# Kernel tuning notes

Measured on AMD Instinct MI355X. Metric: run time of the kernel, lower is better.

## Reference

```python
import jax, jax.numpy as jnp
import numpy as np

N = 50000
IN_CH = 64
HID_CH = 32
NEG_SLOPE = 0.2  # PyG GATConv default for attention LeakyReLU


def _glorot(key, shape):
    fan = shape[0] + shape[-1] if len(shape) > 1 else shape[0]
    s = jnp.sqrt(6.0 / fan)
    return jax.random.uniform(key, shape, jnp.float32, -s, s)


def setup_inputs() -> dict:
    key = jax.random.key(0)
    ks = jax.random.split(key, 20)
    x = jax.random.normal(ks[0], (N, IN_CH), jnp.float32)
    edge_index = jax.random.randint(ks[1], (2, 800000), 0, N, jnp.int64)
    dims = [(IN_CH, IN_CH), (IN_CH, HID_CH), (HID_CH, IN_CH), (IN_CH, IN_CH)]
    inp = {"x": x, "edge_index": edge_index}
    for i, (di, do) in enumerate(dims, 1):
        inp[f"w{i}"] = _glorot(ks[4 * i - 2], (di, do))
        inp[f"as{i}"] = _glorot(ks[4 * i - 1], (do,))
        inp[f"ad{i}"] = _glorot(ks[4 * i], (do,))
        inp[f"b{i}"] = jnp.zeros((do,), jnp.float32)
    return inp


def _gat_layer(x, src, dst, W, a_src, a_dst, b):
    # x: [N, di] -> h: [N, do]
    h = x @ W
    # per-edge attention logits (source + destination contributions)
    e = jax.nn.leaky_relu(h[src] @ a_src + h[dst] @ a_dst, NEG_SLOPE)  # [E]
    # numerically stable segment softmax over incoming edges per dst node
    m = jax.ops.segment_max(e, dst, num_segments=N)
    ex = jnp.exp(e - m[dst])
    denom = jax.ops.segment_sum(ex, dst, num_segments=N)
    alpha = ex / (denom[dst] + 1e-16)  # [E]
    out = jax.ops.segment_sum(alpha[:, None] * h[src], dst, num_segments=N)
    return out + b


def reference(x, edge_index, w1, as1, ad1, b1, w2, as2, ad2, b2,
              w3, as3, ad3, b3, w4, as4, ad4, b4):
    # PyG GATConv adds self-loops by default
    ar = jnp.arange(N, dtype=edge_index.dtype)
    src = jnp.concatenate([edge_index[0], ar])
    dst = jnp.concatenate([edge_index[1], ar])

    h1 = jax.nn.relu(_gat_layer(x, src, dst, w1, as1, ad1, b1))
    h = _gat_layer(h1, src, dst, w2, as2, ad2, b2)
    h3 = jax.nn.relu(h)
    h4 = jax.nn.relu(_gat_layer(h3, src, dst, w3, as3, ad3, b3))
    out = _gat_layer(h4, src, dst, w4, as4, ad4, b4)
    return (out, h)
```

## Files before the change

kernel.cpp:

```cpp
#include <hip/hip_runtime.h>
#include <hip/hip_fp16.h>
#include <math.h>

#define N_NODES 50000
#define N_EDGES 800000
#define E_TOT   850000
#define NEG_SLOPE 0.2f
#define NB_SCAN 49

__global__ void csr_init(int* deg) {
    int i = blockIdx.x * blockDim.x + threadIdx.x;
    if (i < N_NODES) deg[i] = 0;
}

__global__ void csr_degree(const int* __restrict__ dst, int* __restrict__ deg,
                           int* __restrict__ rank) {
    int e = blockIdx.x * blockDim.x + threadIdx.x;
    if (e >= E_TOT) return;
    int d = (e < N_EDGES) ? dst[e] : (e - N_EDGES);
    rank[e] = atomicAdd(&deg[d], 1);
}

__global__ void scan_p1(const int* __restrict__ deg, int* __restrict__ bsum) {
    __shared__ int red[1024];
    int i = blockIdx.x * 1024 + threadIdx.x;
    red[threadIdx.x] = (i < N_NODES) ? deg[i] : 0;
    __syncthreads();
    for (int off = 512; off >= 1; off >>= 1) {
        if (threadIdx.x < off) red[threadIdx.x] += red[threadIdx.x + off];
        __syncthreads();
    }
    if (threadIdx.x == 0) bsum[blockIdx.x] = red[0];
}

__global__ void scan_p3(const int* __restrict__ deg, const int* __restrict__ bsum,
                        int* __restrict__ offs) {
    __shared__ int s[1024];
    __shared__ int bofs;
    int i = blockIdx.x * 1024 + threadIdx.x;
    int v = (i < N_NODES) ? deg[i] : 0;
    s[threadIdx.x] = v;
    if (threadIdx.x < 64) {
        int d = (threadIdx.x < NB_SCAN) ? bsum[threadIdx.x] : 0;
        int p = d;
        for (int off = 1; off < 64; off <<= 1) {
            int u = __shfl_up(p, off, 64);
            if ((int)threadIdx.x >= off) p += u;
        }
        if ((int)threadIdx.x == (int)blockIdx.x) bofs = p - d;
        if (blockIdx.x == NB_SCAN - 1 && threadIdx.x == NB_SCAN - 1)
            offs[N_NODES] = p;
    }
    __syncthreads();
    for (int off = 1; off < 1024; off <<= 1) {
        int u = (threadIdx.x >= off) ? s[threadIdx.x - off] : 0;
        __syncthreads();
        s[threadIdx.x] += u;
        __syncthreads();
    }
    if (i < N_NODES) offs[i] = bofs + s[threadIdx.x] - v;
}

__global__ void csr_fill(const int* __restrict__ src, const int* __restrict__ dst,
                         const int* __restrict__ rank, const int* __restrict__ offs,
                         int* __restrict__ csr_src) {
    int e = blockIdx.x * blockDim.x + threadIdx.x;
    if (e >= E_TOT) return;
    int s, d;
    if (e < N_EDGES) { s = src[e]; d = dst[e]; } else { s = e - N_EDGES; d = s; }
    csr_src[offs[d] + rank[e]] = s;
}

template<int DI, int DO>
__global__ void gemm_proj(const float* __restrict__ X, const float* __restrict__ W,
                          const float* __restrict__ a_src, const float* __restrict__ a_dst,
                          __half* __restrict__ Hh, float* __restrict__ ssrc,
                          float* __restrict__ sdst) {
    const int TPN = DO / 4;
    const int NPB = 256 / TPN;
    __shared__ float sW[DI * DO];
    __shared__ float sX[NPB][DI + 1];
    const int tid = threadIdx.x;
    for (int i = tid; i < DI * DO / 4; i += 256)
        ((float4*)sW)[i] = ((const float4*)W)[i];
    const int base = blockIdx.x * NPB;
    for (int i = tid; i < NPB * DI; i += 256) {
        int r = i / DI, col = i % DI;
        int node = base + r;
        sX[r][col] = (node < N_NODES) ? X[(long)node * DI + col] : 0.0f;
    }
    __syncthreads();
    const int cq = tid % TPN;
    const int g  = tid / TPN;
    const int node = base + g;
    if (node >= N_NODES) return;
    float ax = 0.0f, ay = 0.0f, az = 0.0f, aw = 0.0f;
    const float4* sW4 = (const float4*)sW;
#pragma unroll
    for (int k = 0; k < DI; k++) {
        float xv = sX[g][k];
        float4 w4 = sW4[k * TPN + cq];
        ax = fmaf(xv, w4.x, ax); ay = fmaf(xv, w4.y, ay);
        az = fmaf(xv, w4.z, az); aw = fmaf(xv, w4.w, aw);
    }
    union { uint2 u; __half2 h2[2]; } pk;
    pk.h2[0] = __float22half2_rn(make_float2(ax, ay));
    pk.h2[1] = __float22half2_rn(make_float2(az, aw));
    ((uint2*)(Hh + (long)node * DO))[cq] = pk.u;

    float4 as4 = ((const float4*)a_src)[cq];
    float4 ad4 = ((const float4*)a_dst)[cq];
    float ps = ax * as4.x + ay * as4.y + az * as4.z + aw * as4.w;
    float pd = ax * ad4.x + ay * ad4.y + az * ad4.z + aw * ad4.w;
#pragma unroll
    for (int m = TPN / 2; m >= 1; m >>= 1) {
        ps += __shfl_xor(ps, m, TPN);
        pd += __shfl_xor(pd, m, TPN);
    }
    if (cq == 0) { ssrc[node] = ps; sdst[node] = pd; }
}

template<int DO>
__global__ void gather(const __half* __restrict__ Hh, const float* __restrict__ ssrc,
                       const float* __restrict__ sdst, const int* __restrict__ offs,
                       const int* __restrict__ csr_src, const float* __restrict__ bias,
                       float* __restrict__ feat_out, float* __restrict__ extra_out,
                       int do_relu) {
    const int G = DO / 4;
    const int t = threadIdx.x;
    const int node = blockIdx.x * (256 / G) + t / G;
    const int r = t % G;
    if (node >= N_NODES) return;
    const int beg = offs[node], end = offs[node + 1];
    const float sdv = sdst[node];
    const uint2* H2 = (const uint2*)Hh;

    float4 acc = make_float4(0.0f, 0.0f, 0.0f, 0.0f);
    float den = 0.0f;
    for (int cb = beg; cb < end; cb += G) {
        const int cnt = min(G, end - cb);
        int s0 = 0; float ex = 0.0f;
        if (r < cnt) {
            s0 = csr_src[cb + r];
            float v = ssrc[s0] + sdv;
            v = (v > 0.0f) ? v : NEG_SLOPE * v;
            ex = __expf(v);
        }
        den += ex;
        int j = 0;
        for (; j + 4 <= cnt; j += 4) {
            int   sa = __shfl(s0, j,     G), sb = __shfl(s0, j + 1, G);
            int   sc = __shfl(s0, j + 2, G), sd2 = __shfl(s0, j + 3, G);
            float ea = __shfl(ex, j,     G), eb = __shfl(ex, j + 1, G);
            float ec = __shfl(ex, j + 2, G), ed = __shfl(ex, j + 3, G);
            union { uint2 u; __half2 h2[2]; } ua, ub, uc, ud;
            ua.u = H2[(long)sa * G + r];
            ub.u = H2[(long)sb * G + r];
            uc.u = H2[(long)sc * G + r];
            ud.u = H2[(long)sd2 * G + r];
            float2 a0 = __half22float2(ua.h2[0]), a1 = __half22float2(ua.h2[1]);
            float2 b0 = __half22float2(ub.h2[0]), b1 = __half22float2(ub.h2[1]);
            float2 c0 = __half22float2(uc.h2[0]), c1 = __half22float2(uc.h2[1]);
            float2 d0 = __half22float2(ud.h2[0]), d1 = __half22float2(ud.h2[1]);
            acc.x = fmaf(ea, a0.x, acc.x); acc.y = fmaf(ea, a0.y, acc.y);
            acc.z = fmaf(ea, a1.x, acc.z); acc.w = fmaf(ea, a1.y, acc.w);
            acc.x = fmaf(eb, b0.x, acc.x); acc.y = fmaf(eb, b0.y, acc.y);
            acc.z = fmaf(eb, b1.x, acc.z); acc.w = fmaf(eb, b1.y, acc.w);
            acc.x = fmaf(ec, c0.x, acc.x); acc.y = fmaf(ec, c0.y, acc.y);
            acc.z = fmaf(ec, c1.x, acc.z); acc.w = fmaf(ec, c1.y, acc.w);
            acc.x = fmaf(ed, d0.x, acc.x); acc.y = fmaf(ed, d0.y, acc.y);
            acc.z = fmaf(ed, d1.x, acc.z); acc.w = fmaf(ed, d1.y, acc.w);
        }
        for (; j < cnt; j++) {
            int   sa = __shfl(s0, j, G);
            float ea = __shfl(ex, j, G);
            union { uint2 u; __half2 h2[2]; } ua;
            ua.u = H2[(long)sa * G + r];
            float2 a0 = __half22float2(ua.h2[0]), a1 = __half22float2(ua.h2[1]);
            acc.x = fmaf(ea, a0.x, acc.x); acc.y = fmaf(ea, a0.y, acc.y);
            acc.z = fmaf(ea, a1.x, acc.z); acc.w = fmaf(ea, a1.y, acc.w);
        }
    }
#pragma unroll
    for (int m = G / 2; m >= 1; m >>= 1) den += __shfl_xor(den, m, G);

    float inv = 1.0f / (den + 1e-16f);
    float4 b4 = ((const float4*)bias)[r];
    float4 o;
    o.x = acc.x * inv + b4.x; o.y = acc.y * inv + b4.y;
    o.z = acc.z * inv + b4.z; o.w = acc.w * inv + b4.w;
    long idx = (long)node * G + r;
    if (extra_out) ((float4*)extra_out)[idx] = o;
    if (feat_out) {
        if (do_relu) {
            o.x = fmaxf(o.x, 0.0f); o.y = fmaxf(o.y, 0.0f);
            o.z = fmaxf(o.z, 0.0f); o.w = fmaxf(o.w, 0.0f);
        }
        ((float4*)feat_out)[idx] = o;
    }
}

template<int DI, int DO>
static void run_layer(const float* in_feat, const float* W, const float* a_src,
                      const float* a_dst, const float* b, int do_relu,
                      __half* Hh, float* SS, float* SD,
                      const int* offs, const int* csr_src,
                      float* feat_out, float* extra_out, hipStream_t stream) {
    const int TPN = DO / 4;
    const int NPB = 256 / TPN;
    gemm_proj<DI, DO><<<(N_NODES + NPB - 1) / NPB, 256, 0, stream>>>(
        in_feat, W, a_src, a_dst, Hh, SS, SD);
    const int G = DO / 4;
    const int GNPB = 256 / G;
    gather<DO><<<(N_NODES + GNPB - 1) / GNPB, 256, 0, stream>>>(
        Hh, SS, SD, offs, csr_src, b, feat_out, extra_out, do_relu);
}

extern "C" void kernel_launch(void* const* d_in, const int* in_sizes, int n_in,
                              void* d_out, int out_size, void* d_ws, size_t ws_size,
                              hipStream_t stream) {
    const float* x  = (const float*)d_in[0];
    const int*   ei = (const int*)d_in[1];

    const float* w1  = (const float*)d_in[2];
    const float* as1 = (const float*)d_in[3];
    const float* ad1 = (const float*)d_in[4];
    const float* b1  = (const float*)d_in[5];
    const float* w2  = (const float*)d_in[6];
    const float* as2 = (const float*)d_in[7];
    const float* ad2 = (const float*)d_in[8];
    const float* b2  = (const float*)d_in[9];
    const float* w3  = (const float*)d_in[10];
    const float* as3 = (const float*)d_in[11];
    const float* ad3 = (const float*)d_in[12];
    const float* b3  = (const float*)d_in[13];
    const float* w4  = (const float*)d_in[14];
    const float* as4 = (const float*)d_in[15];
    const float* ad4 = (const float*)d_in[16];
    const float* b4  = (const float*)d_in[17];

    float* out_final = (float*)d_out;
    float* out_h     = (float*)d_out + N_NODES * 64;

    float* ws   = (float*)d_ws;
    __half* Hh  = (__half*)ws;
    float* FEAT = ws + N_NODES * 32;
    float* SS   = FEAT + N_NODES * 64;
    float* SD   = SS + N_NODES;
    int* deg     = (int*)(SD + N_NODES);
    int* rank    = deg + N_NODES;
    int* offs    = rank + E_TOT;
    int* csr_src = offs + N_NODES + 1;
    int* bsum    = csr_src + E_TOT;

    const int* src = ei;
    const int* dst = ei + N_EDGES;

    csr_init<<<(N_NODES + 255) / 256, 256, 0, stream>>>(deg);
    csr_degree<<<(E_TOT + 255) / 256, 256, 0, stream>>>(dst, deg, rank);
    scan_p1<<<NB_SCAN, 1024, 0, stream>>>(deg, bsum);
    scan_p3<<<NB_SCAN, 1024, 0, stream>>>(deg, bsum, offs);
    csr_fill<<<(E_TOT + 255) / 256, 256, 0, stream>>>(src, dst, rank, offs, csr_src);

    run_layer<64, 64>(x, w1, as1, ad1, b1, 1, Hh, SS, SD, offs, csr_src, FEAT, nullptr, stream);
    run_layer<64, 32>(FEAT, w2, as2, ad2, b2, 1, Hh, SS, SD, offs, csr_src, FEAT, out_h, stream);
    run_layer<32, 64>(FEAT, w3, as3, ad3, b3, 1, Hh, SS, SD, offs, csr_src, FEAT, nullptr, stream);
    run_layer<64, 64>(FEAT, w4, as4, ad4, b4, 0, Hh, SS, SD, offs, csr_src, nullptr, out_final, stream);
}
```

Baseline: 291.9 us.

## Fuse each layer's aggregation with the next layer's projection GEMM

Merges the gather/softmax aggregation of layer k with the dense projection and attention-score computation of layer k+1 in a single kernel. The next layer's weight matrix is staged in LDS, and the aggregated row is broadcast across the node's thread group via shuffles. This removes the fp32 intermediate feature write and re-read between layers and cuts three kernel launches. Hidden buffers are now double-buffered as fp16 plus score arrays. The cost is extra LDS use and more register pressure in the gather kernel.

```diff
diff --git a/kernel.cpp b/kernel.cpp
--- a/kernel.cpp
+++ b/kernel.cpp
@@ -120,20 +120,36 @@
     if (cq == 0) { ssrc[node] = ps; sdst[node] = pd; }
 }
 
-template<int DO>
-__global__ void gather(const __half* __restrict__ Hh, const float* __restrict__ ssrc,
-                       const float* __restrict__ sdst, const int* __restrict__ offs,
-                       const int* __restrict__ csr_src, const float* __restrict__ bias,
-                       float* __restrict__ feat_out, float* __restrict__ extra_out,
-                       int do_relu) {
-    const int G = DO / 4;
+template<int DIN, int DOUT>
+__global__ void gather_gemm(const __half* __restrict__ Hh_in,
+                            const float* __restrict__ ssrc_in,
+                            const float* __restrict__ sdst_in,
+                            const int* __restrict__ offs,
+                            const int* __restrict__ csr_src,
+                            const float* __restrict__ bias_in,
+                            int relu_o, float* __restrict__ extra_out,
+                            const float* __restrict__ W2,
+                            const float* __restrict__ a_src2,
+                            const float* __restrict__ a_dst2,
+                            __half* __restrict__ Hh_out,
+                            float* __restrict__ ssrc2, float* __restrict__ sdst2) {
+    const int G = DIN / 4;
+    const int NPB = 256 / G;
+    constexpr int LDSW = (DOUT > 0) ? DIN * DOUT : 1;
+    __shared__ float sW[LDSW];
+    if constexpr (DOUT > 0) {
+        for (int i = threadIdx.x; i < DIN * DOUT / 4; i += 256)
+            ((float4*)sW)[i] = ((const float4*)W2)[i];
+        __syncthreads();
+    }
     const int t = threadIdx.x;
-    const int node = blockIdx.x * (256 / G) + t / G;
+    const int node = blockIdx.x * NPB + t / G;
     const int r = t % G;
-    if (node >= N_NODES) return;
-    const int beg = offs[node], end = offs[node + 1];
-    const float sdv = sdst[node];
-    const uint2* H2 = (const uint2*)Hh;
+    const bool valid = (node < N_NODES);
+    const int beg = valid ? offs[node] : 0;
+    const int end = valid ? offs[node + 1] : 0;
+    const float sdv = valid ? sdst_in[node] : 0.0f;
+    const uint2* H2 = (const uint2*)Hh_in;
 
     float4 acc = make_float4(0.0f, 0.0f, 0.0f, 0.0f);
     float den = 0.0f;
@@ -142,7 +158,7 @@
         int s0 = 0; float ex = 0.0f;
         if (r < cnt) {
             s0 = csr_src[cb + r];
-            float v = ssrc[s0] + sdv;
+            float v = ssrc_in[s0] + sdv;
             v = (v > 0.0f) ? v : NEG_SLOPE * v;
             ex = __expf(v);
         }
@@ -185,35 +201,65 @@
     for (int m = G / 2; m >= 1; m >>= 1) den += __shfl_xor(den, m, G);
 
     float inv = 1.0f / (den + 1e-16f);
-    float4 b4 = ((const float4*)bias)[r];
+    float4 b4 = ((const float4*)bias_in)[r];
     float4 o;
     o.x = acc.x * inv + b4.x; o.y = acc.y * inv + b4.y;
     o.z = acc.z * inv + b4.z; o.w = acc.w * inv + b4.w;
-    long idx = (long)node * G + r;
-    if (extra_out) ((float4*)extra_out)[idx] = o;
-    if (feat_out) {
-        if (do_relu) {
-            o.x = fmaxf(o.x, 0.0f); o.y = fmaxf(o.y, 0.0f);
-            o.z = fmaxf(o.z, 0.0f); o.w = fmaxf(o.w, 0.0f);
-        }
-        ((float4*)feat_out)[idx] = o;
-    }
-}
-
-template<int DI, int DO>
-static void run_layer(const float* in_feat, const float* W, const float* a_src,
-                      const float* a_dst, const float* b, int do_relu,
-                      __half* Hh, float* SS, float* SD,
-                      const int* offs, const int* csr_src,
-                      float* feat_out, float* extra_out, hipStream_t stream) {
-    const int TPN = DO / 4;
-    const int NPB = 256 / TPN;
-    gemm_proj<DI, DO><<<(N_NODES + NPB - 1) / NPB, 256, 0, stream>>>(
-        in_feat, W, a_src, a_dst, Hh, SS, SD);
-    const int G = DO / 4;
-    const int GNPB = 256 / G;
-    gather<DO><<<(N_NODES + GNPB - 1) / GNPB, 256, 0, stream>>>(
-        Hh, SS, SD, offs, csr_src, b, feat_out, extra_out, do_relu);
+    if (valid && extra_out) ((float4*)extra_out)[(long)node * G + r] = o;
+    if (relu_o) {
+        o.x = fmaxf(o.x, 0.0f); o.y = fmaxf(o.y, 0.0f);
+        o.z = fmaxf(o.z, 0.0f); o.w = fmaxf(o.w, 0.0f);
+    }
+
+    if constexpr (DOUT > 0) {
+        constexpr int C = DOUT / (DIN / 4);
+        float acc2[C];
+#pragma unroll
+        for (int c = 0; c < C; c++) acc2[c] = 0.0f;
+        const int cbase = r * C;
+#pragma unroll
+        for (int kb = 0; kb < G; kb++) {
+            float4 o4;
+            o4.x = __shfl(o.x, kb, G);
+            o4.y = __shfl(o.y, kb, G);
+            o4.z = __shfl(o.z, kb, G);
+            o4.w = __shfl(o.w, kb, G);
+            const float* wr = &sW[(4 * kb) * DOUT + cbase];
+#pragma unroll
+            for (int c = 0; c < C; c++) acc2[c] = fmaf(o4.x, wr[c], acc2[c]);
+            wr += DOUT;
+#pragma unroll
+            for (int c = 0; c < C; c++) acc2[c] = fmaf(o4.y, wr[c], acc2[c]);
+            wr += DOUT;
+#pragma unroll
+            for (int c = 0; c < C; c++) acc2[c] = fmaf(o4.z, wr[c], acc2[c]);
+            wr += DOUT;
+#pragma unroll
+            for (int c = 0; c < C; c++) acc2[c] = fmaf(o4.w, wr[c], acc2[c]);
+        }
+        float ps = 0.0f, pd = 0.0f;
+#pragma unroll
+        for (int c = 0; c < C; c++) {
+            ps = fmaf(acc2[c], a_src2[cbase + c], ps);
+            pd = fmaf(acc2[c], a_dst2[cbase + c], pd);
+        }
+#pragma unroll
+        for (int m = G / 2; m >= 1; m >>= 1) {
+            ps += __shfl_xor(ps, m, G);
+            pd += __shfl_xor(pd, m, G);
+        }
+        if (valid) {
+            union { unsigned int u1; uint2 u2; uint4 u4; __half2 h[C / 2]; } pk;
+#pragma unroll
+            for (int c = 0; c < C; c += 2)
+                pk.h[c / 2] = __float22half2_rn(make_float2(acc2[c], acc2[c + 1]));
+            char* dp = (char*)(Hh_out + (long)node * DOUT + cbase);
+            if constexpr (C == 2) *(unsigned int*)dp = pk.u1;
+            else if constexpr (C == 4) *(uint2*)dp = pk.u2;
+            else                        *(uint4*)dp = pk.u4;
+            if (r == 0) { ssrc2[node] = ps; sdst2[node] = pd; }
+        }
+    }
 }
 
 extern "C" void kernel_launch(void* const* d_in, const int* in_sizes, int n_in,
@@ -242,12 +288,14 @@
     float* out_final = (float*)d_out;
     float* out_h     = (float*)d_out + N_NODES * 64;
 
-    float* ws   = (float*)d_ws;
-    __half* Hh  = (__half*)ws;
-    float* FEAT = ws + N_NODES * 32;
-    float* SS   = FEAT + N_NODES * 64;
-    float* SD   = SS + N_NODES;
-    int* deg     = (int*)(SD + N_NODES);
+    float* ws    = (float*)d_ws;
+    __half* Hh_a = (__half*)ws;
+    __half* Hh_b = (__half*)(ws + N_NODES * 32);
+    float* SS_a  = ws + 2 * N_NODES * 32;
+    float* SD_a  = SS_a + N_NODES;
+    float* SS_b  = SD_a + N_NODES;
+    float* SD_b  = SS_b + N_NODES;
+    int* deg     = (int*)(SD_b + N_NODES);
     int* rank    = deg + N_NODES;
     int* offs    = rank + E_TOT;
     int* csr_src = offs + N_NODES + 1;
@@ -262,8 +310,19 @@
     scan_p3<<<NB_SCAN, 1024, 0, stream>>>(deg, bsum, offs);
     csr_fill<<<(E_TOT + 255) / 256, 256, 0, stream>>>(src, dst, rank, offs, csr_src);
 
-    run_layer<64, 64>(x, w1, as1, ad1, b1, 1, Hh, SS, SD, offs, csr_src, FEAT, nullptr, stream);
-    run_layer<64, 32>(FEAT, w2, as2, ad2, b2, 1, Hh, SS, SD, offs, csr_src, FEAT, out_h, stream);
-    run_layer<32, 64>(FEAT, w3, as3, ad3, b3, 1, Hh, SS, SD, offs, csr_src, FEAT, nullptr, stream);
-    run_layer<64, 64>(FEAT, w4, as4, ad4, b4, 0, Hh, SS, SD, offs, csr_src, nullptr, out_final, stream);
-}
+    gemm_proj<64, 64><<<(N_NODES + 15) / 16, 256, 0, stream>>>(
+        x, w1, as1, ad1, Hh_a, SS_a, SD_a);
+
+    gather_gemm<64, 32><<<(N_NODES * 16 + 255) / 256, 256, 0, stream>>>(
+        Hh_a, SS_a, SD_a, offs, csr_src, b1, 1, nullptr,
+        w2, as2, ad2, Hh_b, SS_b, SD_b);
+    gather_gemm<32, 64><<<(N_NODES * 8 + 255) / 256, 256, 0, stream>>>(
+        Hh_b, SS_b, SD_b, offs, csr_src, b2, 1, out_h,
+        w3, as3, ad3, Hh_a, SS_a, SD_a);
+    gather_gemm<64, 64><<<(N_NODES * 16 + 255) / 256, 256, 0, stream>>>(
+        Hh_a, SS_a, SD_a, offs, csr_src, b3, 1, nullptr,
+        w4, as4, ad4, Hh_b, SS_b, SD_b);
+    gather_gemm<64, 0><<<(N_NODES * 16 + 255) / 256, 256, 0, stream>>>(
+        Hh_b, SS_b, SD_b, offs, csr_src, b4, 0, out_final,
+        nullptr, nullptr, nullptr, nullptr, nullptr, nullptr);
+}
```

After: 279.9 us. 1.04x faster.
